# Optimization experiments

Hardware: AMD Instinct MI355X
Metric: run time of the kernel (lower is better)

The kernel has to match this reference:

```python
import jax, jax.numpy as jnp
import numpy as np

QD, KD, HID, NH = 256, 320, 256, 8
NQ, NK, NB = 4096, 4096, 16
DH = HID // NH
EPS = 1e-5
SCALE = float(1.0 / np.sqrt(DH))


def setup_inputs() -> dict:
    key = jax.random.key(0)
    ks = jax.random.split(key, 12)
    s = 0.02
    return {
        "query_nodes": jax.random.normal(ks[0], (NQ, QD), jnp.float32),
        "key_nodes": jax.random.normal(ks[1], (NK, KD), jnp.float32),
        "Wq": jax.random.normal(ks[2], (QD, HID), jnp.float32) * s,
        "bq": jnp.zeros((HID,), jnp.float32),
        "Wk": jax.random.normal(ks[3], (KD, HID), jnp.float32) * s,
        "bk": jnp.zeros((HID,), jnp.float32),
        "Wv": jax.random.normal(ks[4], (KD, HID), jnp.float32) * s,
        "bv": jnp.zeros((HID,), jnp.float32),
        "in_proj_w": jax.random.normal(ks[5], (3 * HID, HID), jnp.float32) * s,
        "in_proj_b": jnp.zeros((3 * HID,), jnp.float32),
        "mha_ow": jax.random.normal(ks[6], (HID, HID), jnp.float32) * s,
        "mha_ob": jnp.zeros((HID,), jnp.float32),
        "Wo": jax.random.normal(ks[7], (HID, QD), jnp.float32) * s,
        "bo": jnp.zeros((QD,), jnp.float32),
        "ln_g": jnp.ones((QD,), jnp.float32),
        "ln_b": jnp.zeros((QD,), jnp.float32),
        "query_batch_idx": jnp.sort(jax.random.randint(ks[8], (NQ,), 0, NB, jnp.int32)),
        "key_batch_idx": jnp.sort(jax.random.randint(ks[9], (NK,), 0, NB, jnp.int32)),
    }


def reference(query_nodes, key_nodes, Wq, bq, Wk, bk, Wv, bv, in_proj_w, in_proj_b,
              mha_ow, mha_ob, Wo, bo, ln_g, ln_b, query_batch_idx, key_batch_idx):
    # outer projections
    q = query_nodes @ Wq + bq          # [NQ, HID]
    k = key_nodes @ Wk + bk            # [NK, HID]
    v = key_nodes @ Wv + bv            # [NK, HID]
    # nn.MultiheadAttention internal in_proj (weights stored [3H, H], applied as x @ W.T)
    q2 = q @ in_proj_w[:HID].T + in_proj_b[:HID]
    k2 = k @ in_proj_w[HID:2 * HID].T + in_proj_b[HID:2 * HID]
    v2 = v @ in_proj_w[2 * HID:].T + in_proj_b[2 * HID:]
    qh = q2.reshape(NQ, NH, DH)
    kh = k2.reshape(NK, NH, DH)
    vh = v2.reshape(NK, NH, DH)
    scores = jnp.einsum('qhd,khd->hqk', qh, kh) * SCALE   # [NH, NQ, NK]
    mask = query_batch_idx[:, None] != key_batch_idx[None, :]  # True = disallowed
    scores = jnp.where(mask[None], -jnp.inf, scores)
    attn = jax.nn.softmax(scores, axis=-1)
    ctx = jnp.einsum('hqk,khd->qhd', attn, vh).reshape(NQ, HID)
    ctx = ctx @ mha_ow + mha_ob        # MHA internal out_proj
    out = ctx @ Wo + bo                # module out_proj back to query_dim
    x = query_nodes + out              # residual (dropout is identity in eval)
    mu = jnp.mean(x, axis=-1, keepdims=True)
    var = jnp.mean((x - mu) ** 2, axis=-1, keepdims=True)
    return (x - mu) / jnp.sqrt(var + EPS) * ln_g + ln_b
```

## Files before the change

### kernel.cpp

```cpp
#include <hip/hip_runtime.h>
#include <hip/hip_bf16.h>
#include <math.h>

#define NQ 4096
#define NK 4096
#define QD 256
#define KD 320
#define HID 256
#define NH 8
#define DH 32
#define NB 16
#define LN_EPS 1e-5f
#define ATT_SCALE 0.17677669529663687f

typedef unsigned short ushort_t;
typedef __attribute__((ext_vector_type(8))) short bf16x8_t;
typedef __attribute__((ext_vector_type(4))) short bf16x4_t;
typedef __attribute__((ext_vector_type(4))) float f32x4_t;

#define OFF_Q2B   0
#define OFF_K2B   524288
#define OFF_V2B   1048576
#define OFF_CTXB  1572864
#define OFF_WQT   2097152
#define OFF_WKT   2129920
#define OFF_WVT   2170880
#define OFF_WOT   2211840
#define OFF_BEFF  2244608
#define OFF_KST   2245632
#define OFF_KEN   2245648
#define OFF_FLAG  2245664

struct KArgs {
    const void* in[18];
    float* ws;
    void* out;
};

__device__ __forceinline__ float bf16_bits_to_f(ushort_t s) {
    unsigned int u = (unsigned int)s << 16;
    float f;
    __builtin_memcpy(&f, &u, 4);
    return f;
}

__device__ __forceinline__ ushort_t f_to_bf16_bits(float v) {
    __hip_bfloat16 t = (__hip_bfloat16)v;
    ushort_t b;
    __builtin_memcpy(&b, &t, 2);
    return b;
}

template <bool F32>
__device__ __forceinline__ bf16x8_t ld8(const void* p, size_t idx) {
    if constexpr (!F32) {
        return *(const bf16x8_t*)((const ushort_t*)p + idx);
    } else {
        f32x4_t f0 = *(const f32x4_t*)((const float*)p + idx);
        f32x4_t f1 = *(const f32x4_t*)((const float*)p + idx + 4);
        bf16x8_t h;
#pragma unroll
        for (int e = 0; e < 4; ++e) h[e] = (short)f_to_bf16_bits(f0[e]);
#pragma unroll
        for (int e = 0; e < 4; ++e) h[4 + e] = (short)f_to_bf16_bits(f1[e]);
        return h;
    }
}

template <bool F32>
__device__ __forceinline__ float ld1f(const void* p, size_t idx) {
    if constexpr (F32) return ((const float*)p)[idx];
    else               return bf16_bits_to_f(((const ushort_t*)p)[idx]);
}

template <bool F32>
__device__ __forceinline__ ushort_t ld1h(const void* p, size_t idx) {
    if constexpr (F32) return f_to_bf16_bits(((const float*)p)[idx]);
    else               return ((const ushort_t*)p)[idx];
}

__device__ __forceinline__ int detect_flag(const void* probe_v, int tid) {
    __shared__ float s_red[4];
    const ushort_t* probe = (const ushort_t*)probe_v;
    float mx = 0.f;
    for (int i = tid; i < 4096; i += 256) {
        float f = fabsf(bf16_bits_to_f(probe[i]));
        if (!(f == f)) f = 1e38f;
        mx = fmaxf(mx, f);
    }
    for (int off = 32; off; off >>= 1) mx = fmaxf(mx, __shfl_xor(mx, off, 64));
    if ((tid & 63) == 0) s_red[tid >> 6] = mx;
    __syncthreads();
    float m2 = fmaxf(fmaxf(s_red[0], s_red[1]), fmaxf(s_red[2], s_red[3]));
    __syncthreads();
    return (m2 < 100.f) ? 1 : 0;
}

template <bool F32>
__device__ __forceinline__ void fuse_qkv_tile(const void* A, size_t abase,
                                              const void* B, ushort_t* Out,
                                              int N, int m0, int n0,
                                              int col, int quad) {
    f32x4_t acc[4];
#pragma unroll
    for (int t = 0; t < 4; ++t) acc[t] = (f32x4_t){0.f, 0.f, 0.f, 0.f};
    size_t aoff = abase + (size_t)(m0 + col) * 256 + quad * 8;
    size_t boff = (size_t)(n0 + col) * 256 + quad * 8;
#pragma unroll
    for (int kc = 0; kc < 256; kc += 32) {
        bf16x8_t af = ld8<F32>(A, aoff + kc);
#pragma unroll
        for (int t = 0; t < 4; ++t) {
            bf16x8_t bf = ld8<F32>(B, boff + (size_t)t * 16 * 256 + kc);
            acc[t] = __builtin_amdgcn_mfma_f32_16x16x32_bf16(af, bf, acc[t], 0, 0, 0);
        }
    }
#pragma unroll
    for (int t = 0; t < 4; ++t)
#pragma unroll
        for (int rr = 0; rr < 4; ++rr)
            Out[(size_t)(m0 + quad * 4 + rr) * N + n0 + t * 16 + col] =
                f_to_bf16_bits(acc[t][rr]);
}

template <bool F32>
__device__ __forceinline__ void fuse_o_tile(const void* Wo, const void* Mow,
                                            ushort_t* Out, int m0, int n0,
                                            int col, int quad) {
    f32x4_t acc[4];
#pragma unroll
    for (int t = 0; t < 4; ++t) acc[t] = (f32x4_t){0.f, 0.f, 0.f, 0.f};
#pragma unroll
    for (int kc = 0; kc < 256; kc += 32) {
        bf16x8_t af;
#pragma unroll
        for (int t = 0; t < 8; ++t)
            af[t] = (short)ld1h<F32>(Wo, (size_t)(kc + quad * 8 + t) * 256 + m0 + col);
#pragma unroll
        for (int t = 0; t < 4; ++t) {
            bf16x8_t bf = ld8<F32>(Mow, (size_t)(n0 + t * 16 + col) * 256 + quad * 8 + kc);
            acc[t] = __builtin_amdgcn_mfma_f32_16x16x32_bf16(af, bf, acc[t], 0, 0, 0);
        }
    }
#pragma unroll
    for (int t = 0; t < 4; ++t)
#pragma unroll
        for (int rr = 0; rr < 4; ++rr)
            Out[(size_t)(m0 + quad * 4 + rr) * 256 + n0 + t * 16 + col] =
                f_to_bf16_bits(acc[t][rr]);
}

template <bool F32>
__device__ __forceinline__ void bias_body(KArgs& a, float* ws, int m, int tid) {
    __shared__ float bsh[256];
    float* beff = ws + OFF_BEFF;
    if (m < 3) {
        const void* bsrc = (m == 0) ? a.in[3] : (m == 1) ? a.in[5] : a.in[7];
        bsh[tid] = ld1f<F32>(bsrc, tid);
        __syncthreads();
        float acc = 0.f;
        size_t row = (size_t)(m * 256 + tid) * 256;
#pragma unroll 4
        for (int kc = 0; kc < 256; kc += 8) {
            bf16x8_t wr = ld8<F32>(a.in[8], row + kc);
#pragma unroll
            for (int t = 0; t < 8; ++t)
                acc += bsh[kc + t] * bf16_bits_to_f((ushort_t)wr[t]);
        }
        acc += ld1f<F32>(a.in[9], m * 256 + tid);
        beff[m * 256 + tid] = acc;
    } else {
        bsh[tid] = ld1f<F32>(a.in[11], tid);
        __syncthreads();
        float acc = 0.f;
        for (int k = 0; k < 256; ++k)
            acc += bsh[k] * ld1f<F32>(a.in[12], (size_t)k * 256 + tid);
        acc += ld1f<F32>(a.in[13], tid);
        beff[3 * 256 + tid] = acc;
    }
}

__global__ __launch_bounds__(256) void k_fuse(KArgs a) {
    float* ws = a.ws;
    const int tid = threadIdx.x, bid = blockIdx.x;
    const int lane = tid & 63, wv = tid >> 6;
    const int col = lane & 15, quad = lane >> 4;
    int fl = detect_flag(a.in[0], tid);
    if (bid == 0 && tid == 0) *(int*)(ws + OFF_FLAG) = fl;

    if (bid < 16) {
        const int* kb = (const int*)a.in[17];
        int* kstart = (int*)(ws + OFF_KST);
        int* kend   = (int*)(ws + OFF_KEN);
        int j = bid * 256 + tid;
        if (j < NK) {
            int b = kb[j];
            if (j == 0) {
                for (int x = 0; x < b; ++x) { kstart[x] = 0; kend[x] = 0; }
                kstart[b] = 0;
            } else {
                int bp = kb[j - 1];
                if (bp != b) {
                    kend[bp] = j;
                    for (int x = bp + 1; x < b; ++x) { kstart[x] = j; kend[x] = j; }
                    kstart[b] = j;
                }
            }
            if (j == NK - 1) {
                kend[b] = NK;
                for (int x = b + 1; x < NB; ++x) { kstart[x] = NK; kend[x] = NK; }
            }
        }
    } else if (bid < 88) {
        int r = bid - 16;
        const void* A; const void* B; ushort_t* Out;
        size_t abase; int N, mb, nb, typ;
        if (r < 16)      { typ = 0; A = a.in[8]; abase = 0;      B = a.in[2]; Out = (ushort_t*)(ws + OFF_WQT); N = 256; mb = r >> 2; nb = r & 3; }
        else if (r < 36) { typ = 0; int rr = r - 16; A = a.in[8]; abase = 65536;  B = a.in[4]; Out = (ushort_t*)(ws + OFF_WKT); N = 320; mb = rr / 5; nb = rr % 5; }
        else if (r < 56) { typ = 0; int rr = r - 36; A = a.in[8]; abase = 131072; B = a.in[6]; Out = (ushort_t*)(ws + OFF_WVT); N = 320; mb = rr / 5; nb = rr % 5; }
        else             { typ = 1; int rr = r - 56; A = a.in[12]; abase = 0; B = a.in[10]; Out = (ushort_t*)(ws + OFF_WOT); N = 256; mb = rr >> 2; nb = rr & 3; }
        int m0 = mb * 64 + wv * 16, n0 = nb * 64;
        if (typ == 0) {
            if (fl) fuse_qkv_tile<false>(A, abase, B, Out, N, m0, n0, col, quad);
            else    fuse_qkv_tile<true >(A, abase, B, Out, N, m0, n0, col, quad);
        } else {
            if (fl) fuse_o_tile<false>(A, B, Out, m0, n0, col, quad);
            else    fuse_o_tile<true >(A, B, Out, m0, n0, col, quad);
        }
    } else {
        int m = bid - 88;
        if (fl) bias_body<false>(a, ws, m, tid);
        else    bias_body<true >(a, ws, m, tid);
    }
}

template <bool F32, int KK>
__device__ __forceinline__ void proj_body(const void* X, const ushort_t* WT,
                                          const float* bias, ushort_t* Z,
                                          int m0, int n0, int col, int quad) {
    f32x4_t acc[4];
#pragma unroll
    for (int t = 0; t < 4; ++t) acc[t] = (f32x4_t){0.f, 0.f, 0.f, 0.f};
    size_t aoff = (size_t)(m0 + col) * KK + quad * 8;
    const ushort_t* Wrow = WT + (size_t)(n0 + col) * KK + quad * 8;
#pragma unroll
    for (int kc = 0; kc < KK; kc += 32) {
        bf16x8_t af = ld8<F32>(X, aoff + kc);
#pragma unroll
        for (int t = 0; t < 4; ++t) {
            bf16x8_t bf = *(const bf16x8_t*)(Wrow + (size_t)t * 16 * KK + kc);
            acc[t] = __builtin_amdgcn_mfma_f32_16x16x32_bf16(af, bf, acc[t], 0, 0, 0);
        }
    }
#pragma unroll
    for (int t = 0; t < 4; ++t)
#pragma unroll
        for (int rr = 0; rr < 4; ++rr) {
            int n = n0 + t * 16 + col;
            Z[(size_t)(m0 + quad * 4 + rr) * 256 + n] =
                f_to_bf16_bits(acc[t][rr] + bias[n]);
        }
}

__global__ __launch_bounds__(256) void k_qkv(KArgs a) {
    float* ws = a.ws;
    const int tid = threadIdx.x, u = blockIdx.x;
    const int lane = tid & 63, wv = tid >> 6;
    const int col = lane & 15, quad = lane >> 4;
    const int fl = *(const int*)(ws + OFF_FLAG);
    const float* beff = ws + OFF_BEFF;

    if (u < 256) {
        int m0 = (u >> 2) * 64 + wv * 16, n0 = (u & 3) * 64;
        const ushort_t* WT = (const ushort_t*)(ws + OFF_WQT);
        ushort_t* Z = (ushort_t*)(ws + OFF_Q2B);
        if (fl) proj_body<false, 256>(a.in[0], WT, beff, Z, m0, n0, col, quad);
        else    proj_body<true , 256>(a.in[0], WT, beff, Z, m0, n0, col, quad);
    } else if (u < 512) {
        int uu = u - 256;
        int m0 = (uu >> 2) * 64 + wv * 16, n0 = (uu & 3) * 64;
        const ushort_t* WT = (const ushort_t*)(ws + OFF_WKT);
        ushort_t* Z = (ushort_t*)(ws + OFF_K2B);
        if (fl) proj_body<false, 320>(a.in[1], WT, beff + 256, Z, m0, n0, col, quad);
        else    proj_body<true , 320>(a.in[1], WT, beff + 256, Z, m0, n0, col, quad);
    } else {
        int uu = u - 512;
        int m0 = (uu >> 2) * 64 + wv * 16, n0 = (uu & 3) * 64;
        const ushort_t* WT = (const ushort_t*)(ws + OFF_WVT);
        ushort_t* Z = (ushort_t*)(ws + OFF_V2B);
        if (fl) proj_body<false, 320>(a.in[1], WT, beff + 512, Z, m0, n0, col, quad);
        else    proj_body<true , 320>(a.in[1], WT, beff + 512, Z, m0, n0, col, quad);
    }
}

__global__ __launch_bounds__(256) void k_attn(KArgs a) {
    float* ws = a.ws;
    const ushort_t* q2b = (const ushort_t*)(ws + OFF_Q2B);
    const ushort_t* k2b = (const ushort_t*)(ws + OFF_K2B);
    const ushort_t* v2b = (const ushort_t*)(ws + OFF_V2B);
    const int* qb  = (const int*)a.in[16];
    const int* kst = (const int*)(ws + OFF_KST);
    const int* ken = (const int*)(ws + OFF_KEN);
    ushort_t* ctxb = (ushort_t*)(ws + OFF_CTXB);

    int wave = threadIdx.x >> 6;
    int lane = threadIdx.x & 63;
    int qt = blockIdx.x >> 1;
    int h  = ((blockIdx.x & 1) << 2) | wave;
    int q0 = qt * 16;
    int col  = lane & 15;
    int quad = lane >> 4;

    int qq = q0 + col;
    int bq_ = qb[qq];
    int j0q = kst[bq_], j1q = ken[bq_];
    int jlo = j0q, jhi = j1q;
#pragma unroll
    for (int off = 1; off < 16; off <<= 1) {
        jlo = min(jlo, __shfl_xor(jlo, off, 64));
        jhi = max(jhi, __shfl_xor(jhi, off, 64));
    }

    bf16x8_t qf = *(const bf16x8_t*)(q2b + (size_t)qq * HID + h * DH + quad * 8);

    f32x4_t accO  = {0.f, 0.f, 0.f, 0.f};
    f32x4_t accO2 = {0.f, 0.f, 0.f, 0.f};
    float l_st = 0.f;

    for (int kt = jlo; kt < jhi; kt += 32) {
        int ktB = kt + 16;
        int krowA = kt + col;   if (krowA > NK - 1) krowA = NK - 1;
        int krowB = ktB + col;  if (krowB > NK - 1) krowB = NK - 1;
        bf16x8_t kfA = *(const bf16x8_t*)(k2b + (size_t)krowA * HID + h * DH + quad * 8);
        bf16x8_t kfB = *(const bf16x8_t*)(k2b + (size_t)krowB * HID + h * DH + quad * 8);
        ushort_t vrA[4], vrB[4];
#pragma unroll
        for (int j = 0; j < 4; ++j) {
            int vrowA = kt + quad * 4 + j;   if (vrowA > NK - 1) vrowA = NK - 1;
            int vrowB = ktB + quad * 4 + j;  if (vrowB > NK - 1) vrowB = NK - 1;
            vrA[j] = v2b[(size_t)vrowA * HID + h * DH + col];
            vrB[j] = v2b[(size_t)vrowB * HID + h * DH + col];
        }
        f32x4_t SA = __builtin_amdgcn_mfma_f32_16x16x32_bf16(
            kfA, qf, (f32x4_t){0.f, 0.f, 0.f, 0.f}, 0, 0, 0);
        f32x4_t SB = __builtin_amdgcn_mfma_f32_16x16x32_bf16(
            kfB, qf, (f32x4_t){0.f, 0.f, 0.f, 0.f}, 0, 0, 0);

        bf16x4_t pbA, vbA, pbB, vbB;
#pragma unroll
        for (int r = 0; r < 4; ++r) {
            int kkA = kt + quad * 4 + r;
            bool okA = (kkA >= j0q) && (kkA < j1q);
            float pA = okA ? __expf(SA[r] * ATT_SCALE) : 0.f;
            l_st += pA;
            pbA[r] = (short)f_to_bf16_bits(pA);
            vbA[r] = (short)vrA[r];
            int kkB = ktB + quad * 4 + r;
            bool okB = (kkB >= j0q) && (kkB < j1q);
            float pB = okB ? __expf(SB[r] * ATT_SCALE) : 0.f;
            l_st += pB;
            pbB[r] = (short)f_to_bf16_bits(pB);
            vbB[r] = (short)vrB[r];
        }
        accO  = __builtin_amdgcn_mfma_f32_16x16x16bf16_1k(pbA, vbA, accO,  0, 0, 0);
        accO2 = __builtin_amdgcn_mfma_f32_16x16x16bf16_1k(pbB, vbB, accO2, 0, 0, 0);
    }
#pragma unroll
    for (int r = 0; r < 4; ++r) accO[r] += accO2[r];

    l_st += __shfl_xor(l_st, 16, 64);
    l_st += __shfl_xor(l_st, 32, 64);

#pragma unroll
    for (int r = 0; r < 4; ++r) {
        int qrow_local = quad * 4 + r;
        float lq = __shfl(l_st, qrow_local, 64);
        float o = (lq > 0.f) ? accO[r] / lq : 0.f;
        int qrow = q0 + qrow_local;
        ctxb[(size_t)qrow * HID + h * DH + col] = f_to_bf16_bits(o);
    }
}

template <bool F32>
__device__ __forceinline__ void oln_body(KArgs& a, float* ws, int u,
                                         int wv, int col, int quad, int fl) {
    __shared__ float sred[4][16], ssred[4][16];
    const ushort_t* ctxb = (const ushort_t*)(ws + OFF_CTXB);
    const ushort_t* wot  = (const ushort_t*)(ws + OFF_WOT);
    const float* beffO = ws + OFF_BEFF + 3 * 256;

    int m0 = u * 16;
    f32x4_t acc[4];
#pragma unroll
    for (int t = 0; t < 4; ++t) acc[t] = (f32x4_t){0.f, 0.f, 0.f, 0.f};
    const ushort_t* Xrow = ctxb + (size_t)(m0 + col) * 256 + quad * 8;
    const ushort_t* Wbase = wot + (size_t)col * 256 + quad * 8;
#pragma unroll
    for (int kc = 0; kc < 256; kc += 32) {
        bf16x8_t af = *(const bf16x8_t*)(Xrow + kc);
#pragma unroll
        for (int tt = 0; tt < 4; ++tt) {
            int t = wv * 4 + tt;
            bf16x8_t bf = *(const bf16x8_t*)(Wbase + (size_t)t * 16 * 256 + kc);
            acc[tt] = __builtin_amdgcn_mfma_f32_16x16x32_bf16(af, bf, acc[tt], 0, 0, 0);
        }
    }
    float s_[4] = {0.f, 0.f, 0.f, 0.f};
    float ss_[4] = {0.f, 0.f, 0.f, 0.f};
#pragma unroll
    for (int tt = 0; tt < 4; ++tt) {
        int n = (wv * 4 + tt) * 16 + col;
        float b = beffO[n];
#pragma unroll
        for (int rr = 0; rr < 4; ++rr) {
            int m = m0 + quad * 4 + rr;
            float x = acc[tt][rr] + b + ld1f<F32>(a.in[0], (size_t)m * 256 + n);
            acc[tt][rr] = x;
            s_[rr] += x;
            ss_[rr] += x * x;
        }
    }
#pragma unroll
    for (int off = 1; off < 16; off <<= 1) {
#pragma unroll
        for (int rr = 0; rr < 4; ++rr) {
            s_[rr]  += __shfl_xor(s_[rr],  off, 16);
            ss_[rr] += __shfl_xor(ss_[rr], off, 16);
        }
    }
    if (col == 0) {
#pragma unroll
        for (int rr = 0; rr < 4; ++rr) {
            sred[wv][quad * 4 + rr]  = s_[rr];
            ssred[wv][quad * 4 + rr] = ss_[rr];
        }
    }
    __syncthreads();
    float mu[4], inv[4];
#pragma unroll
    for (int rr = 0; rr < 4; ++rr) {
        int row = quad * 4 + rr;
        float ts  = sred[0][row]  + sred[1][row]  + sred[2][row]  + sred[3][row];
        float tss = ssred[0][row] + ssred[1][row] + ssred[2][row] + ssred[3][row];
        mu[rr] = ts * (1.f / QD);
        float var = tss * (1.f / QD) - mu[rr] * mu[rr];
        inv[rr] = rsqrtf(var + LN_EPS);
    }
#pragma unroll
    for (int tt = 0; tt < 4; ++tt) {
        int n = (wv * 4 + tt) * 16 + col;
        float g = ld1f<F32>(a.in[14], n), bb = ld1f<F32>(a.in[15], n);
#pragma unroll
        for (int rr = 0; rr < 4; ++rr) {
            int m = m0 + quad * 4 + rr;
            float y = (acc[tt][rr] - mu[rr]) * inv[rr] * g + bb;
            size_t idx = (size_t)m * 256 + n;
            if (fl) ((ushort_t*)a.out)[idx] = f_to_bf16_bits(y);
            else    ((float*)a.out)[idx] = y;
        }
    }
}

__global__ __launch_bounds__(256) void k_oln(KArgs a) {
    float* ws = a.ws;
    const int tid = threadIdx.x;
    const int lane = tid & 63, wv = tid >> 6;
    const int col = lane & 15, quad = lane >> 4;
    const int fl = *(const int*)(ws + OFF_FLAG);
    if (fl) oln_body<false>(a, ws, blockIdx.x, wv, col, quad, fl);
    else    oln_body<true >(a, ws, blockIdx.x, wv, col, quad, fl);
}

extern "C" void kernel_launch(void* const* d_in, const int* in_sizes, int n_in,
                              void* d_out, int out_size, void* d_ws, size_t ws_size,
                              hipStream_t stream) {
    KArgs a;
    for (int i = 0; i < 18; ++i) a.in[i] = d_in[i];
    a.ws = (float*)d_ws;
    a.out = d_out;

    k_fuse<<<92, 256, 0, stream>>>(a);
    k_qkv<<<768, 256, 0, stream>>>(a);
    k_attn<<<512, 256, 0, stream>>>(a);
    k_oln<<<256, 256, 0, stream>>>(a);
}
```

Before: 148.3 us.

## Fuse attention and output projection with LayerNorm into one kernel

Merges the attention kernel and the output-projection/residual/LayerNorm kernel into a single 512-thread kernel. Each block handles 16 queries across all 8 heads, one wave per head, and keeps the context tile in shared memory. That removes one launch and the global write and re-read of the context buffer. In exchange each wave now computes only two 16-column output tiles in the projection, and the LayerNorm reduction spans 8 waves. A leftover preload of the stale context buffer from global memory into shared memory adds a small wasted read.

```diff
diff --git a/kernel.cpp b/kernel.cpp
--- a/kernel.cpp
+++ b/kernel.cpp
@@ -293,182 +293,188 @@
     }
 }
 
-__global__ __launch_bounds__(256) void k_attn(KArgs a) {
+#define CTXP 264
+
+template <bool F32>
+__device__ __forceinline__ void oln_part(KArgs& a, float* ws,
+                                         const ushort_t ctxl[16][CTXP],
+                                         float sred[8][16], float ssred[8][16],
+                                         int q0, int wv, int col, int quad,
+                                         int fl) {
+    const ushort_t* wot  = (const ushort_t*)(ws + OFF_WOT);
+    const float* beffO = ws + OFF_BEFF + 3 * 256;
+
+    f32x4_t acc[2];
+#pragma unroll
+    for (int t = 0; t < 2; ++t) acc[t] = (f32x4_t){0.f, 0.f, 0.f, 0.f};
+    const ushort_t* Wbase = wot + (size_t)col * 256 + quad * 8;
+#pragma unroll
+    for (int kc = 0; kc < 256; kc += 32) {
+        bf16x8_t af = *(const bf16x8_t*)(&ctxl[col][quad * 8 + kc]);
+#pragma unroll
+        for (int tt = 0; tt < 2; ++tt) {
+            int t = wv * 2 + tt;
+            bf16x8_t bf = *(const bf16x8_t*)(Wbase + (size_t)t * 16 * 256 + kc);
+            acc[tt] = __builtin_amdgcn_mfma_f32_16x16x32_bf16(af, bf, acc[tt], 0, 0, 0);
+        }
+    }
+    float s_[4] = {0.f, 0.f, 0.f, 0.f};
+    float ss_[4] = {0.f, 0.f, 0.f, 0.f};
+#pragma unroll
+    for (int tt = 0; tt < 2; ++tt) {
+        int n = (wv * 2 + tt) * 16 + col;
+        float b = beffO[n];
+#pragma unroll
+        for (int rr = 0; rr < 4; ++rr) {
+            int m = q0 + quad * 4 + rr;
+            float x = acc[tt][rr] + b + ld1f<F32>(a.in[0], (size_t)m * 256 + n);
+            acc[tt][rr] = x;
+            s_[rr] += x;
+            ss_[rr] += x * x;
+        }
+    }
+#pragma unroll
+    for (int off = 1; off < 16; off <<= 1) {
+#pragma unroll
+        for (int rr = 0; rr < 4; ++rr) {
+            s_[rr]  += __shfl_xor(s_[rr],  off, 16);
+            ss_[rr] += __shfl_xor(ss_[rr], off, 16);
+        }
+    }
+    if (col == 0) {
+#pragma unroll
+        for (int rr = 0; rr < 4; ++rr) {
+            sred[wv][quad * 4 + rr]  = s_[rr];
+            ssred[wv][quad * 4 + rr] = ss_[rr];
+        }
+    }
+    __syncthreads();
+    float mu[4], inv[4];
+#pragma unroll
+    for (int rr = 0; rr < 4; ++rr) {
+        int row = quad * 4 + rr;
+        float ts = 0.f, tss = 0.f;
+#pragma unroll
+        for (int w = 0; w < 8; ++w) { ts += sred[w][row]; tss += ssred[w][row]; }
+        mu[rr] = ts * (1.f / QD);
+        float var = tss * (1.f / QD) - mu[rr] * mu[rr];
+        inv[rr] = rsqrtf(var + LN_EPS);
+    }
+#pragma unroll
+    for (int tt = 0; tt < 2; ++tt) {
+        int n = (wv * 2 + tt) * 16 + col;
+        float g = ld1f<F32>(a.in[14], n), bb = ld1f<F32>(a.in[15], n);
+#pragma unroll
+        for (int rr = 0; rr < 4; ++rr) {
+            int m = q0 + quad * 4 + rr;
+            float y = (acc[tt][rr] - mu[rr]) * inv[rr] * g + bb;
+            size_t idx = (size_t)m * 256 + n;
+            if (fl) ((ushort_t*)a.out)[idx] = f_to_bf16_bits(y);
+            else    ((float*)a.out)[idx] = y;
+        }
+    }
+}
+
+__global__ __launch_bounds__(512) void k_attn_oln(KArgs a) {
+    __shared__ ushort_t ctxl[16][CTXP];
+    __shared__ float sred[8][16], ssred[8][16];
     float* ws = a.ws;
     const ushort_t* q2b = (const ushort_t*)(ws + OFF_Q2B);
     const ushort_t* k2b = (const ushort_t*)(ws + OFF_K2B);
     const ushort_t* v2b = (const ushort_t*)(ws + OFF_V2B);
+    const ushort_t* ctxb = (const ushort_t*)(ws + OFF_CTXB);
     const int* qb  = (const int*)a.in[16];
     const int* kst = (const int*)(ws + OFF_KST);
     const int* ken = (const int*)(ws + OFF_KEN);
-    ushort_t* ctxb = (ushort_t*)(ws + OFF_CTXB);
-
-    int wave = threadIdx.x >> 6;
-    int lane = threadIdx.x & 63;
-    int qt = blockIdx.x >> 1;
-    int h  = ((blockIdx.x & 1) << 2) | wave;
-    int q0 = qt * 16;
-    int col  = lane & 15;
-    int quad = lane >> 4;
-
-    int qq = q0 + col;
-    int bq_ = qb[qq];
-    int j0q = kst[bq_], j1q = ken[bq_];
-    int jlo = j0q, jhi = j1q;
-#pragma unroll
-    for (int off = 1; off < 16; off <<= 1) {
-        jlo = min(jlo, __shfl_xor(jlo, off, 64));
-        jhi = max(jhi, __shfl_xor(jhi, off, 64));
-    }
-
-    bf16x8_t qf = *(const bf16x8_t*)(q2b + (size_t)qq * HID + h * DH + quad * 8);
-
-    f32x4_t accO  = {0.f, 0.f, 0.f, 0.f};
-    f32x4_t accO2 = {0.f, 0.f, 0.f, 0.f};
-    float l_st = 0.f;
-
-    for (int kt = jlo; kt < jhi; kt += 32) {
-        int ktB = kt + 16;
-        int krowA = kt + col;   if (krowA > NK - 1) krowA = NK - 1;
-        int krowB = ktB + col;  if (krowB > NK - 1) krowB = NK - 1;
-        bf16x8_t kfA = *(const bf16x8_t*)(k2b + (size_t)krowA * HID + h * DH + quad * 8);
-        bf16x8_t kfB = *(const bf16x8_t*)(k2b + (size_t)krowB * HID + h * DH + quad * 8);
-        ushort_t vrA[4], vrB[4];
-#pragma unroll
-        for (int j = 0; j < 4; ++j) {
-            int vrowA = kt + quad * 4 + j;   if (vrowA > NK - 1) vrowA = NK - 1;
-            int vrowB = ktB + quad * 4 + j;  if (vrowB > NK - 1) vrowB = NK - 1;
-            vrA[j] = v2b[(size_t)vrowA * HID + h * DH + col];
-            vrB[j] = v2b[(size_t)vrowB * HID + h * DH + col];
-        }
-        f32x4_t SA = __builtin_amdgcn_mfma_f32_16x16x32_bf16(
-            kfA, qf, (f32x4_t){0.f, 0.f, 0.f, 0.f}, 0, 0, 0);
-        f32x4_t SB = __builtin_amdgcn_mfma_f32_16x16x32_bf16(
-            kfB, qf, (f32x4_t){0.f, 0.f, 0.f, 0.f}, 0, 0, 0);
-
-        bf16x4_t pbA, vbA, pbB, vbB;
-#pragma unroll
-        for (int r = 0; r < 4; ++r) {
-            int kkA = kt + quad * 4 + r;
-            bool okA = (kkA >= j0q) && (kkA < j1q);
-            float pA = okA ? __expf(SA[r] * ATT_SCALE) : 0.f;
-            l_st += pA;
-            pbA[r] = (short)f_to_bf16_bits(pA);
-            vbA[r] = (short)vrA[r];
-            int kkB = ktB + quad * 4 + r;
-            bool okB = (kkB >= j0q) && (kkB < j1q);
-            float pB = okB ? __expf(SB[r] * ATT_SCALE) : 0.f;
-            l_st += pB;
-            pbB[r] = (short)f_to_bf16_bits(pB);
-            vbB[r] = (short)vrB[r];
-        }
-        accO  = __builtin_amdgcn_mfma_f32_16x16x16bf16_1k(pbA, vbA, accO,  0, 0, 0);
-        accO2 = __builtin_amdgcn_mfma_f32_16x16x16bf16_1k(pbB, vbB, accO2, 0, 0, 0);
-    }
-#pragma unroll
-    for (int r = 0; r < 4; ++r) accO[r] += accO2[r];
-
-    l_st += __shfl_xor(l_st, 16, 64);
-    l_st += __shfl_xor(l_st, 32, 64);
-
-#pragma unroll
-    for (int r = 0; r < 4; ++r) {
-        int qrow_local = quad * 4 + r;
-        float lq = __shfl(l_st, qrow_local, 64);
-        float o = (lq > 0.f) ? accO[r] / lq : 0.f;
-        int qrow = q0 + qrow_local;
-        ctxb[(size_t)qrow * HID + h * DH + col] = f_to_bf16_bits(o);
-    }
-}
-
-template <bool F32>
-__device__ __forceinline__ void oln_body(KArgs& a, float* ws, int u,
-                                         int wv, int col, int quad, int fl) {
-    __shared__ float sred[4][16], ssred[4][16];
-    const ushort_t* ctxb = (const ushort_t*)(ws + OFF_CTXB);
-    const ushort_t* wot  = (const ushort_t*)(ws + OFF_WOT);
-    const float* beffO = ws + OFF_BEFF + 3 * 256;
-
-    int m0 = u * 16;
-    f32x4_t acc[4];
-#pragma unroll
-    for (int t = 0; t < 4; ++t) acc[t] = (f32x4_t){0.f, 0.f, 0.f, 0.f};
-    const ushort_t* Xrow = ctxb + (size_t)(m0 + col) * 256 + quad * 8;
-    const ushort_t* Wbase = wot + (size_t)col * 256 + quad * 8;
-#pragma unroll
-    for (int kc = 0; kc < 256; kc += 32) {
-        bf16x8_t af = *(const bf16x8_t*)(Xrow + kc);
-#pragma unroll
-        for (int tt = 0; tt < 4; ++tt) {
-            int t = wv * 4 + tt;
-            bf16x8_t bf = *(const bf16x8_t*)(Wbase + (size_t)t * 16 * 256 + kc);
-            acc[tt] = __builtin_amdgcn_mfma_f32_16x16x32_bf16(af, bf, acc[tt], 0, 0, 0);
-        }
-    }
-    float s_[4] = {0.f, 0.f, 0.f, 0.f};
-    float ss_[4] = {0.f, 0.f, 0.f, 0.f};
-#pragma unroll
-    for (int tt = 0; tt < 4; ++tt) {
-        int n = (wv * 4 + tt) * 16 + col;
-        float b = beffO[n];
-#pragma unroll
-        for (int rr = 0; rr < 4; ++rr) {
-            int m = m0 + quad * 4 + rr;
-            float x = acc[tt][rr] + b + ld1f<F32>(a.in[0], (size_t)m * 256 + n);
-            acc[tt][rr] = x;
-            s_[rr] += x;
-            ss_[rr] += x * x;
-        }
-    }
-#pragma unroll
-    for (int off = 1; off < 16; off <<= 1) {
-#pragma unroll
-        for (int rr = 0; rr < 4; ++rr) {
-            s_[rr]  += __shfl_xor(s_[rr],  off, 16);
-            ss_[rr] += __shfl_xor(ss_[rr], off, 16);
-        }
-    }
-    if (col == 0) {
-#pragma unroll
-        for (int rr = 0; rr < 4; ++rr) {
-            sred[wv][quad * 4 + rr]  = s_[rr];
-            ssred[wv][quad * 4 + rr] = ss_[rr];
-        }
-    }
-    __syncthreads();
-    float mu[4], inv[4];
-#pragma unroll
-    for (int rr = 0; rr < 4; ++rr) {
-        int row = quad * 4 + rr;
-        float ts  = sred[0][row]  + sred[1][row]  + sred[2][row]  + sred[3][row];
-        float tss = ssred[0][row] + ssred[1][row] + ssred[2][row] + ssred[3][row];
-        mu[rr] = ts * (1.f / QD);
-        float var = tss * (1.f / QD) - mu[rr] * mu[rr];
-        inv[rr] = rsqrtf(var + LN_EPS);
-    }
-#pragma unroll
-    for (int tt = 0; tt < 4; ++tt) {
-        int n = (wv * 4 + tt) * 16 + col;
-        float g = ld1f<F32>(a.in[14], n), bb = ld1f<F32>(a.in[15], n);
-#pragma unroll
-        for (int rr = 0; rr < 4; ++rr) {
-            int m = m0 + quad * 4 + rr;
-            float y = (acc[tt][rr] - mu[rr]) * inv[rr] * g + bb;
-            size_t idx = (size_t)m * 256 + n;
-            if (fl) ((ushort_t*)a.out)[idx] = f_to_bf16_bits(y);
-            else    ((float*)a.out)[idx] = y;
-        }
-    }
-}
-
-__global__ __launch_bounds__(256) void k_oln(KArgs a) {
-    float* ws = a.ws;
+
     const int tid = threadIdx.x;
     const int lane = tid & 63, wv = tid >> 6;
     const int col = lane & 15, quad = lane >> 4;
     const int fl = *(const int*)(ws + OFF_FLAG);
-    if (fl) oln_body<false>(a, ws, blockIdx.x, wv, col, quad, fl);
-    else    oln_body<true >(a, ws, blockIdx.x, wv, col, quad, fl);
+    const int qt = blockIdx.x;
+    const int q0 = qt * 16;
+    const int h  = wv;
+
+    {
+        int m = tid >> 5, nblk = (tid & 31) * 8;
+        *(bf16x8_t*)(&ctxl[m][nblk]) =
+            *(const bf16x8_t*)(ctxb + (size_t)(q0 + m) * 256 + nblk);
+    }
+    __syncthreads();
+
+    {
+        int qq = q0 + col;
+        int bq_ = qb[qq];
+        int j0q = kst[bq_], j1q = ken[bq_];
+        int jlo = j0q, jhi = j1q;
+#pragma unroll
+        for (int off = 1; off < 16; off <<= 1) {
+            jlo = min(jlo, __shfl_xor(jlo, off, 64));
+            jhi = max(jhi, __shfl_xor(jhi, off, 64));
+        }
+
+        bf16x8_t qf = *(const bf16x8_t*)(q2b + (size_t)qq * HID + h * DH + quad * 8);
+
+        f32x4_t accO  = {0.f, 0.f, 0.f, 0.f};
+        f32x4_t accO2 = {0.f, 0.f, 0.f, 0.f};
+        float l_st = 0.f;
+
+        for (int kt = jlo; kt < jhi; kt += 32) {
+            int ktB = kt + 16;
+            int krowA = kt + col;   if (krowA > NK - 1) krowA = NK - 1;
+            int krowB = ktB + col;  if (krowB > NK - 1) krowB = NK - 1;
+            bf16x8_t kfA = *(const bf16x8_t*)(k2b + (size_t)krowA * HID + h * DH + quad * 8);
+            bf16x8_t kfB = *(const bf16x8_t*)(k2b + (size_t)krowB * HID + h * DH + quad * 8);
+            ushort_t vrA[4], vrB[4];
+#pragma unroll
+            for (int j = 0; j < 4; ++j) {
+                int vrowA = kt + quad * 4 + j;   if (vrowA > NK - 1) vrowA = NK - 1;
+                int vrowB = ktB + quad * 4 + j;  if (vrowB > NK - 1) vrowB = NK - 1;
+                vrA[j] = v2b[(size_t)vrowA * HID + h * DH + col];
+                vrB[j] = v2b[(size_t)vrowB * HID + h * DH + col];
+            }
+            f32x4_t SA = __builtin_amdgcn_mfma_f32_16x16x32_bf16(
+                kfA, qf, (f32x4_t){0.f, 0.f, 0.f, 0.f}, 0, 0, 0);
+            f32x4_t SB = __builtin_amdgcn_mfma_f32_16x16x32_bf16(
+                kfB, qf, (f32x4_t){0.f, 0.f, 0.f, 0.f}, 0, 0, 0);
+
+            bf16x4_t pbA, vbA, pbB, vbB;
+#pragma unroll
+            for (int r = 0; r < 4; ++r) {
+                int kkA = kt + quad * 4 + r;
+                bool okA = (kkA >= j0q) && (kkA < j1q);
+                float pA = okA ? __expf(SA[r] * ATT_SCALE) : 0.f;
+                l_st += pA;
+                pbA[r] = (short)f_to_bf16_bits(pA);
+                vbA[r] = (short)vrA[r];
+                int kkB = ktB + quad * 4 + r;
+                bool okB = (kkB >= j0q) && (kkB < j1q);
+                float pB = okB ? __expf(SB[r] * ATT_SCALE) : 0.f;
+                l_st += pB;
+                pbB[r] = (short)f_to_bf16_bits(pB);
+                vbB[r] = (short)vrB[r];
+            }
+            accO  = __builtin_amdgcn_mfma_f32_16x16x16bf16_1k(pbA, vbA, accO,  0, 0, 0);
+            accO2 = __builtin_amdgcn_mfma_f32_16x16x16bf16_1k(pbB, vbB, accO2, 0, 0, 0);
+        }
+#pragma unroll
+        for (int r = 0; r < 4; ++r) accO[r] += accO2[r];
+
+        l_st += __shfl_xor(l_st, 16, 64);
+        l_st += __shfl_xor(l_st, 32, 64);
+
+#pragma unroll
+        for (int r = 0; r < 4; ++r) {
+            int qrow_local = quad * 4 + r;
+            float lq = __shfl(l_st, qrow_local, 64);
+            float o = (lq > 0.f) ? accO[r] / lq : 0.f;
+            ctxl[qrow_local][h * DH + col] = f_to_bf16_bits(o);
+        }
+    }
+    __syncthreads();
+
+    if (fl) oln_part<false>(a, ws, ctxl, sred, ssred, q0, wv, col, quad, fl);
+    else    oln_part<true >(a, ws, ctxl, sred, ssred, q0, wv, col, quad, fl);
 }
 
 extern "C" void kernel_launch(void* const* d_in, const int* in_sizes, int n_in,
@@ -481,6 +487,5 @@
 
     k_fuse<<<92, 256, 0, stream>>>(a);
     k_qkv<<<768, 256, 0, stream>>>(a);
-    k_attn<<<512, 256, 0, stream>>>(a);
-    k_oln<<<256, 256, 0, stream>>>(a);
-}
+    k_attn_oln<<<256, 512, 0, stream>>>(a);
+}
```

After: 145.6 us. No clear change (-1.8%).
